# Kernel optimization log

Measured on AMD Instinct MI355X. Metric: run time of the kernel, lower is better.

The kernel has to match this reference:

```python
import jax, jax.numpy as jnp
import numpy as np
from jax import lax

COMMITMENT_WEIGHT = 0.25
EMA_DECAY = 0.99
EPS = 1e-5


def setup_inputs() -> dict:
    key = jax.random.key(0)
    k1, k2, k3 = jax.random.split(key, 3)
    B, L, D, K = 32, 512, 384, 8192
    z = jax.random.normal(k1, (B, L, D), dtype=jnp.float32)
    codebook = jax.random.normal(k2, (K, D), dtype=jnp.float32)
    ema_cluster_size = jnp.zeros((K,), dtype=jnp.float32)
    ema_embed_sum = jax.random.normal(k3, (K, D), dtype=jnp.float32)
    return {"z": z, "codebook": codebook, "ema_cluster_size": ema_cluster_size, "ema_embed_sum": ema_embed_sum}


def reference(z, codebook, ema_cluster_size, ema_embed_sum):
    B, L, D = z.shape
    K = codebook.shape[0]
    flat_z = z.reshape(-1, D)  # [N, D]

    # squared L2 distance to every code: [N, K]
    dist = (
        jnp.sum(flat_z * flat_z, axis=-1, keepdims=True)
        + jnp.sum(codebook * codebook, axis=-1)[None, :]
        - 2.0 * (flat_z @ codebook.T)
    )
    indices = jnp.argmin(dist, axis=-1)  # [N]
    quantized = codebook[indices].reshape(B, L, D)

    # EMA codebook update (training-mode, no-grad in original)
    cluster_size = jax.ops.segment_sum(jnp.ones_like(indices, dtype=flat_z.dtype), indices, num_segments=K)
    embed_sum = jax.ops.segment_sum(flat_z, indices, num_segments=K)  # [K, D]
    new_cluster_size = ema_cluster_size * EMA_DECAY + (1.0 - EMA_DECAY) * cluster_size
    new_embed_sum = ema_embed_sum * EMA_DECAY + (1.0 - EMA_DECAY) * embed_sum
    n = jnp.sum(new_cluster_size)
    cluster_size_smoothed = (new_cluster_size + EPS) / (n + K * EPS) * n
    new_codebook = new_embed_sum / cluster_size_smoothed[:, None]

    commitment_loss = jnp.mean((z - lax.stop_gradient(quantized)) ** 2)
    codebook_loss = jnp.mean((quantized - lax.stop_gradient(z)) ** 2)
    loss = codebook_loss + COMMITMENT_WEIGHT * commitment_loss

    # straight-through estimator
    quantized_st = z + lax.stop_gradient(quantized - z)
    return (quantized_st, indices.reshape(B, L), loss, new_cluster_size, new_embed_sum, new_codebook)
```

## Files before the change

kernel.cpp:

```cpp
#include <hip/hip_runtime.h>
#include <math.h>

#define N_TOK 16384
#define DDIM  384
#define KCODE 8192
#define EMA   0.99f
#define EPS_F 1e-5f
#define MARGIN 0.5f
#define NB 32

typedef _Float16 f16x8 __attribute__((ext_vector_type(8)));
typedef float    f32x4 __attribute__((ext_vector_type(4)));

#define OFF_PD1    0UL
#define OFF_PI1    2097152UL
#define OFF_PFL    4194304UL
#define OFF_CBH    6291456UL
#define OFF_TOKL   0UL
#define OFF_OFFS   65536UL
#define OFF_CURS   98560UL
#define OFF_WSIDX  12582912UL
#define OFF_COUNTS 12648448UL
#define OFF_SUMSQ  12681216UL
#define OFF_NACC   12681220UL
#define OFF_CNORM  12681472UL
#define OFF_FLIST  12714240UL
#define OFF_FCNT   12779776UL
#define OFF_PSUM   12780032UL
#define OFF_FD1    12796416UL

typedef __attribute__((address_space(1))) const unsigned int gas_uint;
typedef __attribute__((address_space(3))) unsigned int       las_uint;
__device__ __forceinline__ void gload_lds16(const void* g, void* l) {
    __builtin_amdgcn_global_load_lds((gas_uint*)g, (las_uint*)l, 16, 0, 0);
}

__global__ void convert_norm_kernel(const float* __restrict__ z, const float* __restrict__ cb,
                                    _Float16* __restrict__ zh, _Float16* __restrict__ cbh,
                                    float* __restrict__ cnorm,
                                    float* __restrict__ zero_cnts, int* __restrict__ fcnt) {
    if (blockIdx.x == 0) {
        for (int i = threadIdx.x; i < 8256; i += 256) zero_cnts[i] = 0.f;
        if (threadIdx.x < 64) fcnt[threadIdx.x] = 0;
    }
    int row  = (blockIdx.x * blockDim.x + threadIdx.x) >> 6;
    int lane = threadIdx.x & 63;
    const float* src;
    _Float16* dst;
    bool is_cb = (row >= N_TOK);
    if (is_cb) { int k = row - N_TOK; src = cb + (size_t)k * DDIM; dst = cbh + (size_t)k * DDIM; }
    else       {                      src = z  + (size_t)row * DDIM; dst = zh + (size_t)row * DDIM; }
    float s = 0.f;
    #pragma unroll
    for (int r = 0; r < 3; r++) {
        int e = (lane + 64 * r) * 2;
        float2 v = *(const float2*)(src + e);
        s = fmaf(v.x, v.x, fmaf(v.y, v.y, s));
        _Float16 h0 = (_Float16)v.x, h1 = (_Float16)v.y;
        dst[e] = h0; dst[e + 1] = h1;
    }
    if (is_cb) {
        #pragma unroll
        for (int off = 32; off > 0; off >>= 1) s += __shfl_down(s, off, 64);
        if (lane == 0) cnorm[row - N_TOK] = s;
    }
}

__launch_bounds__(512, 4)
__global__ void argmin16_kernel(const _Float16* __restrict__ zh, const _Float16* __restrict__ cbh,
                                const float* __restrict__ cnorm,
                                float* __restrict__ pd1, int* __restrict__ pi1,
                                int* __restrict__ pfl) {
    __shared__ _Float16 As[128 * 64];
    __shared__ _Float16 Bs[256 * 64];

    const int tid  = threadIdx.x;
    const int lane = tid & 63;
    const int wv   = tid >> 6;
    const int wy   = wv >> 2;
    const int wx   = wv & 3;
    const int m0   = blockIdx.x * 128;
    const int n0   = blockIdx.y * 256;
    const int l15  = lane & 15;
    const int l4   = lane >> 4;
    const int rsw  = l15 & 7;

    f32x4 acc[4][4];
    #pragma unroll
    for (int i = 0; i < 4; i++)
        #pragma unroll
        for (int j = 0; j < 4; j++) acc[i][j] = (f32x4){0.f, 0.f, 0.f, 0.f};

    const int r8  = lane >> 3;
    const int jch = (lane & 7) ^ (r8 & 7);
    const _Float16* a_g = zh  + (size_t)(m0 + wv * 8 + r8) * DDIM + jch * 8;
    const _Float16* b_g = cbh + (size_t)(n0 + wv * 8 + r8) * DDIM + jch * 8;
    _Float16* a_d = As + wv * 512;
    _Float16* b_d = Bs + wv * 512;

    gload_lds16(a_g,                      a_d);
    gload_lds16(a_g + (size_t)64 * DDIM,  a_d + 4096);
    gload_lds16(b_g,                      b_d);
    gload_lds16(b_g + (size_t)64 * DDIM,  b_d + 4096);
    gload_lds16(b_g + (size_t)128 * DDIM, b_d + 8192);
    gload_lds16(b_g + (size_t)192 * DDIM, b_d + 12288);

    for (int it = 0; it < 6; it++) {
        __syncthreads();
        f16x8 af[4], bf[4];
        #pragma unroll
        for (int im = 0; im < 4; im++)
            af[im] = *(const f16x8*)(As + (wy * 64 + im * 16 + l15) * 64 + (l4 ^ rsw) * 8);
        #pragma unroll
        for (int in = 0; in < 4; in++)
            bf[in] = *(const f16x8*)(Bs + (wx * 64 + in * 16 + l15) * 64 + (l4 ^ rsw) * 8);
        #pragma unroll
        for (int im = 0; im < 4; im++)
            #pragma unroll
            for (int in = 0; in < 4; in++)
                acc[im][in] = __builtin_amdgcn_mfma_f32_16x16x32_f16(af[im], bf[in], acc[im][in], 0, 0, 0);
        #pragma unroll
        for (int im = 0; im < 4; im++)
            af[im] = *(const f16x8*)(As + (wy * 64 + im * 16 + l15) * 64 + ((4 + l4) ^ rsw) * 8);
        #pragma unroll
        for (int in = 0; in < 4; in++)
            bf[in] = *(const f16x8*)(Bs + (wx * 64 + in * 16 + l15) * 64 + ((4 + l4) ^ rsw) * 8);
        __syncthreads();
        if (it < 5) {
            int kc = (it + 1) * 64;
            gload_lds16(a_g + kc,                      a_d);
            gload_lds16(a_g + (size_t)64 * DDIM + kc,  a_d + 4096);
            gload_lds16(b_g + kc,                      b_d);
            gload_lds16(b_g + (size_t)64 * DDIM + kc,  b_d + 4096);
            gload_lds16(b_g + (size_t)128 * DDIM + kc, b_d + 8192);
            gload_lds16(b_g + (size_t)192 * DDIM + kc, b_d + 12288);
        }
        #pragma unroll
        for (int im = 0; im < 4; im++)
            #pragma unroll
            for (int in = 0; in < 4; in++)
                acc[im][in] = __builtin_amdgcn_mfma_f32_16x16x32_f16(af[im], bf[in], acc[im][in], 0, 0, 0);
    }

    float* xd1 = (float*)&As[0];
    int*   xfl = (int*)(xd1 + 512);
    int*   xi1 = (int*)(xd1 + 1024);

    float cn[4]; int cid[4];
    #pragma unroll
    for (int in = 0; in < 4; in++) {
        cid[in] = n0 + wx * 64 + in * 16 + l15;
        cn[in] = cnorm[cid[in]];
    }
    #pragma unroll
    for (int im = 0; im < 4; im++) {
        #pragma unroll
        for (int reg = 0; reg < 4; reg++) {
            float dd[4];
            #pragma unroll
            for (int in = 0; in < 4; in++) dd[in] = cn[in] - 2.f * acc[im][in][reg];
            float d1 = dd[0]; int i1 = cid[0];
            #pragma unroll
            for (int in = 1; in < 4; in++)
                if (dd[in] < d1) { d1 = dd[in]; i1 = cid[in]; }
            #pragma unroll
            for (int off = 1; off < 16; off <<= 1) {
                float od = __shfl_xor(d1, off, 16);
                int   oi = __shfl_xor(i1, off, 16);
                if (od < d1 || (od == d1 && oi < i1)) { d1 = od; i1 = oi; }
            }
            bool fl = false;
            #pragma unroll
            for (int in = 0; in < 4; in++) fl |= (dd[in] < d1 + MARGIN) && (cid[in] != i1);
            unsigned long long bal = __ballot(fl);
            int gf = ((bal >> (l4 * 16)) & 0xFFFFULL) != 0ULL;
            if (l15 == 0) {
                int tl = wy * 64 + im * 16 + l4 * 4 + reg;
                xd1[tl * 4 + wx] = d1; xi1[tl * 4 + wx] = i1; xfl[tl * 4 + wx] = gf;
            }
        }
    }
    __syncthreads();
    if (tid < 128) {
        float d1 = xd1[tid * 4]; int i1 = xi1[tid * 4]; int fl = xfl[tid * 4];
        #pragma unroll
        for (int x = 1; x < 4; x++) {
            float od = xd1[tid * 4 + x]; int oi = xi1[tid * 4 + x]; int ofl = xfl[tid * 4 + x];
            if (od < d1 || (od == d1 && oi < i1)) { d1 = od; i1 = oi; fl = ofl; }
        }
        #pragma unroll
        for (int x = 0; x < 4; x++) {
            float od = xd1[tid * 4 + x]; int oi = xi1[tid * 4 + x];
            fl |= (oi != i1 && od < d1 + MARGIN) ? 1 : 0;
        }
        size_t o = (size_t)blockIdx.y * N_TOK + m0 + tid;
        pd1[o] = d1; pi1[o] = i1; pfl[o] = fl;
    }
}

__global__ void topmerge_kernel(const float* __restrict__ pd1, const int* __restrict__ pi1,
                                const int* __restrict__ pfl,
                                int* __restrict__ ws_idx, float* __restrict__ out_idx,
                                int* __restrict__ fcnt, int* __restrict__ flist,
                                float* __restrict__ fd1) {
    int t = blockIdx.x * blockDim.x + threadIdx.x;
    if (t >= N_TOK) return;
    float d1 = pd1[t]; int i1 = pi1[t]; int fl = pfl[t];
    float d2 = 3.4e38f;
    for (int nb = 1; nb < NB; nb++) {
        size_t o = (size_t)nb * N_TOK + t;
        float od1 = pd1[o]; int oi1 = pi1[o]; int ofl = pfl[o];
        if (od1 < d1 || (od1 == d1 && oi1 < i1)) { d2 = fminf(d2, d1); d1 = od1; i1 = oi1; fl = ofl; }
        else d2 = fminf(d2, od1);
    }
    ws_idx[t] = i1;
    out_idx[t] = (float)i1;
    fd1[t] = d1;
    if (fl || (d2 - d1 < MARGIN)) {
        int s = atomicAdd(fcnt, 1);
        flist[s] = t;
    }
}

__launch_bounds__(256)
__global__ void rescore2_kernel(const float* __restrict__ z, const float* __restrict__ cb,
                                const float* __restrict__ cnorm,
                                const float* __restrict__ pd1, const float* __restrict__ fd1,
                                const int* __restrict__ flist, const int* __restrict__ fcnt,
                                int* __restrict__ ws_idx, float* __restrict__ out_idx) {
    __shared__ float zt[4 * 384];
    const int lane = threadIdx.x & 63;
    const int wv   = threadIdx.x >> 6;
    const int count = fcnt[0];
    float* zrow = zt + wv * 384;
    for (int slot = blockIdx.x * 4 + wv; slot < count; slot += 2048 * 4) {
        int t = flist[slot];
        const float* zr = z + (size_t)t * DDIM;
        #pragma unroll
        for (int r = 0; r < 6; r++) zrow[lane + 64 * r] = zr[lane + 64 * r];
        float band = fd1[t] + MARGIN;
        float bd = 3.4e38f; int bi = 0x7fffffff;
        for (int nb = 0; nb < NB; nb++) {
            if (pd1[(size_t)nb * N_TOK + t] >= band) continue;
            #pragma unroll
            for (int c4 = 0; c4 < 4; c4++) {
                int c = nb * 256 + c4 * 64 + lane;
                const float* cr = cb + (size_t)c * DDIM;
                float a = 0.f;
                for (int d4 = 0; d4 < 96; d4++) {
                    float4 cv = *(const float4*)(cr + d4 * 4);
                    float4 zv = *(const float4*)(zrow + d4 * 4);
                    a = fmaf(zv.x, cv.x, a);
                    a = fmaf(zv.y, cv.y, a);
                    a = fmaf(zv.z, cv.z, a);
                    a = fmaf(zv.w, cv.w, a);
                }
                float dd = cnorm[c] - 2.f * a;
                if (dd < bd) { bd = dd; bi = c; }
            }
        }
        #pragma unroll
        for (int off = 32; off > 0; off >>= 1) {
            float od = __shfl_xor(bd, off, 64);
            int   oi = __shfl_xor(bi, off, 64);
            if (od < bd || (od == bd && oi < bi)) { bd = od; bi = oi; }
        }
        if (lane == 0) { ws_idx[t] = bi; out_idx[t] = (float)bi; }
    }
}

__global__ void quantize_kernel(const float* __restrict__ z, const float* __restrict__ cb,
                                const int* __restrict__ ws_idx,
                                float* __restrict__ out_q,
                                float* __restrict__ counts, float* __restrict__ psum) {
    __shared__ float sm[4];
    int t = (blockIdx.x * blockDim.x + threadIdx.x) >> 6;
    int lane = threadIdx.x & 63, wv = threadIdx.x >> 6;
    int k = ws_idx[t];
    const float* zr = z + (size_t)t * DDIM;
    const float* cr = cb + (size_t)k * DDIM;
    float* qr = out_q + (size_t)t * DDIM;
    float s = 0.f;
    #pragma unroll
    for (int r = 0; r < 6; r++) {
        int d = lane + 64 * r;
        float zv = zr[d];
        float qv = cr[d];
        qr[d] = qv;
        float df = zv - qv;
        s += df * df;
    }
    #pragma unroll
    for (int off = 32; off > 0; off >>= 1) s += __shfl_down(s, off, 64);
    if (lane == 0) {
        sm[wv] = s;
        atomicAdd(counts + k, 1.0f);
    }
    __syncthreads();
    if (threadIdx.x == 0) psum[blockIdx.x] = sm[0] + sm[1] + sm[2] + sm[3];
}

__global__ void scan_cluster_kernel(const float* __restrict__ counts,
                                    const float* __restrict__ ema_cs,
                                    const float* __restrict__ psum,
                                    int* __restrict__ offs, int* __restrict__ curs,
                                    float* __restrict__ out_ncs, float* __restrict__ n_acc,
                                    float* __restrict__ out_loss) {
    __shared__ int ps[1024];
    __shared__ float red[32];
    const int t = threadIdx.x;
    const int base = t * 8;
    int loc[8]; int s = 0; float cf[8];
    #pragma unroll
    for (int i = 0; i < 8; i++) { cf[i] = counts[base + i]; int c = (int)(cf[i] + 0.5f); loc[i] = s; s += c; }
    ps[t] = s;
    __syncthreads();
    for (int off = 1; off < 1024; off <<= 1) {
        int v = ps[t];
        int add = (t >= off) ? ps[t - off] : 0;
        __syncthreads();
        ps[t] = v + add;
        __syncthreads();
    }
    int excl = (t == 0) ? 0 : ps[t - 1];
    #pragma unroll
    for (int i = 0; i < 8; i++) {
        int o = excl + loc[i];
        offs[base + i] = o;
        curs[base + i] = o;
    }
    if (t == 1023) offs[KCODE] = ps[1023];
    float vs = 0.f;
    #pragma unroll
    for (int i = 0; i < 8; i++) {
        float v = EMA * ema_cs[base + i] + (1.f - EMA) * cf[i];
        out_ncs[base + i] = v;
        vs += v;
    }
    float ls = 0.f;
    for (int j = t; j < 4096; j += 1024) ls += psum[j];
    int lane = t & 63, w = t >> 6;
    #pragma unroll
    for (int off = 32; off > 0; off >>= 1) { vs += __shfl_down(vs, off, 64); ls += __shfl_down(ls, off, 64); }
    if (lane == 0) { red[w] = vs; red[16 + w] = ls; }
    __syncthreads();
    if (t == 0) {
        float n = 0.f, l = 0.f;
        #pragma unroll
        for (int w2 = 0; w2 < 16; w2++) { n += red[w2]; l += red[16 + w2]; }
        n_acc[0] = n;
        out_loss[0] = 1.25f * l / (float)(N_TOK * DDIM);
    }
}

__global__ void fill_kernel(const int* __restrict__ ws_idx,
                            int* __restrict__ curs, int* __restrict__ toklist) {
    int t = blockIdx.x * blockDim.x + threadIdx.x;
    if (t >= N_TOK) return;
    int k = ws_idx[t];
    int slot = atomicAdd(curs + k, 1);
    toklist[slot] = t;
}

__global__ void codebook_fused_kernel(const float* __restrict__ z,
                                      const int* __restrict__ offs, const int* __restrict__ toklist,
                                      const float* __restrict__ ema_es,
                                      const float* __restrict__ ncs, const float* __restrict__ n_acc,
                                      float* __restrict__ out_es, float* __restrict__ out_cb) {
    int k = (blockIdx.x * blockDim.x + threadIdx.x) >> 6;
    int lane = threadIdx.x & 63;
    if (k >= KCODE) return;
    int o0 = offs[k], o1 = offs[k + 1];
    float sum[6] = {0.f, 0.f, 0.f, 0.f, 0.f, 0.f};
    for (int s = o0; s < o1; s++) {
        int tok = toklist[s];
        const float* zr = z + (size_t)tok * DDIM;
        #pragma unroll
        for (int r = 0; r < 6; r++) sum[r] += zr[lane + 64 * r];
    }
    float n = n_acc[0];
    float smooth = (ncs[k] + EPS_F) / (n + (float)KCODE * EPS_F) * n;
    float inv = 1.f / smooth;
    const float* er = ema_es + (size_t)k * DDIM;
    float* oes = out_es + (size_t)k * DDIM;
    float* ocb = out_cb + (size_t)k * DDIM;
    #pragma unroll
    for (int r = 0; r < 6; r++) {
        int d = lane + 64 * r;
        float es = EMA * er[d] + (1.f - EMA) * sum[r];
        oes[d] = es;
        ocb[d] = es * inv;
    }
}

extern "C" void kernel_launch(void* const* d_in, const int* in_sizes, int n_in,
                              void* d_out, int out_size, void* d_ws, size_t ws_size,
                              hipStream_t stream) {
    const float* z       = (const float*)d_in[0];
    const float* cb      = (const float*)d_in[1];
    const float* ema_cs  = (const float*)d_in[2];
    const float* ema_es  = (const float*)d_in[3];

    float* out      = (float*)d_out;
    float* out_q    = out;
    float* out_idx  = out + 6291456;
    float* out_loss = out + 6307840;
    float* out_ncs  = out + 6307841;
    float* out_es   = out + 6316033;
    float* out_cb   = out + 9461761;

    char* w = (char*)d_ws;
    float* pd1    = (float*)(w + OFF_PD1);
    int*   pi1    = (int*)  (w + OFF_PI1);
    int*   pfl    = (int*)  (w + OFF_PFL);
    _Float16* cbh = (_Float16*)(w + OFF_CBH);
    int*   toklist= (int*)  (w + OFF_TOKL);
    int*   offs   = (int*)  (w + OFF_OFFS);
    int*   curs   = (int*)  (w + OFF_CURS);
    float* cnorm  = (float*)(w + OFF_CNORM);
    int*   flist  = (int*)  (w + OFF_FLIST);
    int*   fcnt   = (int*)  (w + OFF_FCNT);
    int*   ws_idx = (int*)  (w + OFF_WSIDX);
    float* counts = (float*)(w + OFF_COUNTS);
    float* psum   = (float*)(w + OFF_PSUM);
    float* n_acc  = (float*)(w + OFF_NACC);
    float* fd1    = (float*)(w + OFF_FD1);

    _Float16* zh = (_Float16*)out;

    convert_norm_kernel<<<(N_TOK + KCODE) / 4, 256, 0, stream>>>(z, cb, zh, cbh, cnorm, counts, fcnt);

    dim3 grid_am(N_TOK / 128, KCODE / 256, 1);
    argmin16_kernel<<<grid_am, 512, 0, stream>>>(zh, cbh, cnorm, pd1, pi1, pfl);

    topmerge_kernel<<<N_TOK / 256, 256, 0, stream>>>(pd1, pi1, pfl, ws_idx, out_idx, fcnt, flist, fd1);

    rescore2_kernel<<<2048, 256, 0, stream>>>(z, cb, cnorm, pd1, fd1, flist, fcnt, ws_idx, out_idx);

    quantize_kernel<<<N_TOK * 64 / 256, 256, 0, stream>>>(z, cb, ws_idx, out_q, counts, psum);
    scan_cluster_kernel<<<1, 1024, 0, stream>>>(counts, ema_cs, psum, offs, curs, out_ncs, n_acc, out_loss);
    fill_kernel<<<N_TOK / 256, 256, 0, stream>>>(ws_idx, curs, toklist);
    codebook_fused_kernel<<<KCODE * 64 / 256, 256, 0, stream>>>(z, offs, toklist, ema_es, out_ncs, n_acc, out_es, out_cb);
}
```

Measured before the change: 550.7 us.

## Fold quantize pass into codebook update and move counts into argmin merge

Removes the separate quantize kernel. Cluster counts are now accumulated with atomics in topmerge for unflagged tokens and in rescore for flagged ones. The quantized output write and the loss sum of squares move into the per-code codebook kernel, which already reads each assigned token's z row, so z is read once fewer. The loss is zeroed in scan and then accumulated with atomics, which makes its summation order nondeterministic. Work per code is now uneven, since codes with many tokens also write all of their quantized rows.

```diff
diff --git a/kernel.cpp b/kernel.cpp
--- a/kernel.cpp
+++ b/kernel.cpp
@@ -26,7 +26,6 @@
 #define OFF_CNORM  12681472UL
 #define OFF_FLIST  12714240UL
 #define OFF_FCNT   12779776UL
-#define OFF_PSUM   12780032UL
 #define OFF_FD1    12796416UL
 
 typedef __attribute__((address_space(1))) const unsigned int gas_uint;
@@ -202,7 +201,7 @@
                                 const int* __restrict__ pfl,
                                 int* __restrict__ ws_idx, float* __restrict__ out_idx,
                                 int* __restrict__ fcnt, int* __restrict__ flist,
-                                float* __restrict__ fd1) {
+                                float* __restrict__ fd1, float* __restrict__ counts) {
     int t = blockIdx.x * blockDim.x + threadIdx.x;
     if (t >= N_TOK) return;
     float d1 = pd1[t]; int i1 = pi1[t]; int fl = pfl[t];
@@ -219,6 +218,8 @@
     if (fl || (d2 - d1 < MARGIN)) {
         int s = atomicAdd(fcnt, 1);
         flist[s] = t;
+    } else {
+        atomicAdd(counts + i1, 1.0f);
     }
 }
 
@@ -227,7 +228,8 @@
                                 const float* __restrict__ cnorm,
                                 const float* __restrict__ pd1, const float* __restrict__ fd1,
                                 const int* __restrict__ flist, const int* __restrict__ fcnt,
-                                int* __restrict__ ws_idx, float* __restrict__ out_idx) {
+                                int* __restrict__ ws_idx, float* __restrict__ out_idx,
+                                float* __restrict__ counts) {
     __shared__ float zt[4 * 384];
     const int lane = threadIdx.x & 63;
     const int wv   = threadIdx.x >> 6;
@@ -265,49 +267,20 @@
             int   oi = __shfl_xor(bi, off, 64);
             if (od < bd || (od == bd && oi < bi)) { bd = od; bi = oi; }
         }
-        if (lane == 0) { ws_idx[t] = bi; out_idx[t] = (float)bi; }
-    }
-}
-
-__global__ void quantize_kernel(const float* __restrict__ z, const float* __restrict__ cb,
-                                const int* __restrict__ ws_idx,
-                                float* __restrict__ out_q,
-                                float* __restrict__ counts, float* __restrict__ psum) {
-    __shared__ float sm[4];
-    int t = (blockIdx.x * blockDim.x + threadIdx.x) >> 6;
-    int lane = threadIdx.x & 63, wv = threadIdx.x >> 6;
-    int k = ws_idx[t];
-    const float* zr = z + (size_t)t * DDIM;
-    const float* cr = cb + (size_t)k * DDIM;
-    float* qr = out_q + (size_t)t * DDIM;
-    float s = 0.f;
-    #pragma unroll
-    for (int r = 0; r < 6; r++) {
-        int d = lane + 64 * r;
-        float zv = zr[d];
-        float qv = cr[d];
-        qr[d] = qv;
-        float df = zv - qv;
-        s += df * df;
-    }
-    #pragma unroll
-    for (int off = 32; off > 0; off >>= 1) s += __shfl_down(s, off, 64);
-    if (lane == 0) {
-        sm[wv] = s;
-        atomicAdd(counts + k, 1.0f);
-    }
-    __syncthreads();
-    if (threadIdx.x == 0) psum[blockIdx.x] = sm[0] + sm[1] + sm[2] + sm[3];
+        if (lane == 0) {
+            ws_idx[t] = bi; out_idx[t] = (float)bi;
+            atomicAdd(counts + bi, 1.0f);
+        }
+    }
 }
 
 __global__ void scan_cluster_kernel(const float* __restrict__ counts,
                                     const float* __restrict__ ema_cs,
-                                    const float* __restrict__ psum,
                                     int* __restrict__ offs, int* __restrict__ curs,
                                     float* __restrict__ out_ncs, float* __restrict__ n_acc,
                                     float* __restrict__ out_loss) {
     __shared__ int ps[1024];
-    __shared__ float red[32];
+    __shared__ float red[16];
     const int t = threadIdx.x;
     const int base = t * 8;
     int loc[8]; int s = 0; float cf[8];
@@ -337,19 +310,17 @@
         out_ncs[base + i] = v;
         vs += v;
     }
-    float ls = 0.f;
-    for (int j = t; j < 4096; j += 1024) ls += psum[j];
     int lane = t & 63, w = t >> 6;
     #pragma unroll
-    for (int off = 32; off > 0; off >>= 1) { vs += __shfl_down(vs, off, 64); ls += __shfl_down(ls, off, 64); }
-    if (lane == 0) { red[w] = vs; red[16 + w] = ls; }
+    for (int off = 32; off > 0; off >>= 1) vs += __shfl_down(vs, off, 64);
+    if (lane == 0) red[w] = vs;
     __syncthreads();
     if (t == 0) {
-        float n = 0.f, l = 0.f;
-        #pragma unroll
-        for (int w2 = 0; w2 < 16; w2++) { n += red[w2]; l += red[16 + w2]; }
+        float n = 0.f;
+        #pragma unroll
+        for (int w2 = 0; w2 < 16; w2++) n += red[w2];
         n_acc[0] = n;
-        out_loss[0] = 1.25f * l / (float)(N_TOK * DDIM);
+        out_loss[0] = 0.f;
     }
 }
 
@@ -362,34 +333,59 @@
     toklist[slot] = t;
 }
 
-__global__ void codebook_fused_kernel(const float* __restrict__ z,
+__global__ void codebook_fused_kernel(const float* __restrict__ z, const float* __restrict__ cb,
                                       const int* __restrict__ offs, const int* __restrict__ toklist,
                                       const float* __restrict__ ema_es,
                                       const float* __restrict__ ncs, const float* __restrict__ n_acc,
-                                      float* __restrict__ out_es, float* __restrict__ out_cb) {
+                                      float* __restrict__ out_q, float* __restrict__ out_es,
+                                      float* __restrict__ out_cb, float* __restrict__ out_loss) {
+    __shared__ float sm[4];
     int k = (blockIdx.x * blockDim.x + threadIdx.x) >> 6;
     int lane = threadIdx.x & 63;
-    if (k >= KCODE) return;
-    int o0 = offs[k], o1 = offs[k + 1];
-    float sum[6] = {0.f, 0.f, 0.f, 0.f, 0.f, 0.f};
-    for (int s = o0; s < o1; s++) {
-        int tok = toklist[s];
-        const float* zr = z + (size_t)tok * DDIM;
-        #pragma unroll
-        for (int r = 0; r < 6; r++) sum[r] += zr[lane + 64 * r];
-    }
-    float n = n_acc[0];
-    float smooth = (ncs[k] + EPS_F) / (n + (float)KCODE * EPS_F) * n;
-    float inv = 1.f / smooth;
-    const float* er = ema_es + (size_t)k * DDIM;
-    float* oes = out_es + (size_t)k * DDIM;
-    float* ocb = out_cb + (size_t)k * DDIM;
-    #pragma unroll
-    for (int r = 0; r < 6; r++) {
-        int d = lane + 64 * r;
-        float es = EMA * er[d] + (1.f - EMA) * sum[r];
-        oes[d] = es;
-        ocb[d] = es * inv;
+    int wv = threadIdx.x >> 6;
+    float sumsq = 0.f;
+    if (k < KCODE) {
+        int o0 = offs[k], o1 = offs[k + 1];
+        float ck[6];
+        const float* cr = cb + (size_t)k * DDIM;
+        #pragma unroll
+        for (int r = 0; r < 6; r++) ck[r] = cr[lane + 64 * r];
+        float sum[6] = {0.f, 0.f, 0.f, 0.f, 0.f, 0.f};
+        for (int s = o0; s < o1; s++) {
+            int tok = toklist[s];
+            const float* zr = z + (size_t)tok * DDIM;
+            float* qr = out_q + (size_t)tok * DDIM;
+            #pragma unroll
+            for (int r = 0; r < 6; r++) {
+                int d = lane + 64 * r;
+                float zv = zr[d];
+                sum[r] += zv;
+                float df = zv - ck[r];
+                sumsq = fmaf(df, df, sumsq);
+                qr[d] = ck[r];
+            }
+        }
+        float n = n_acc[0];
+        float smooth = (ncs[k] + EPS_F) / (n + (float)KCODE * EPS_F) * n;
+        float inv = 1.f / smooth;
+        const float* er = ema_es + (size_t)k * DDIM;
+        float* oes = out_es + (size_t)k * DDIM;
+        float* ocb = out_cb + (size_t)k * DDIM;
+        #pragma unroll
+        for (int r = 0; r < 6; r++) {
+            int d = lane + 64 * r;
+            float es = EMA * er[d] + (1.f - EMA) * sum[r];
+            oes[d] = es;
+            ocb[d] = es * inv;
+        }
+    }
+    #pragma unroll
+    for (int off = 32; off > 0; off >>= 1) sumsq += __shfl_down(sumsq, off, 64);
+    if (lane == 0) sm[wv] = sumsq;
+    __syncthreads();
+    if (threadIdx.x == 0) {
+        float b = sm[0] + sm[1] + sm[2] + sm[3];
+        atomicAdd(out_loss, 1.25f * b / (float)(N_TOK * DDIM));
     }
 }
 
@@ -422,7 +418,6 @@
     int*   fcnt   = (int*)  (w + OFF_FCNT);
     int*   ws_idx = (int*)  (w + OFF_WSIDX);
     float* counts = (float*)(w + OFF_COUNTS);
-    float* psum   = (float*)(w + OFF_PSUM);
     float* n_acc  = (float*)(w + OFF_NACC);
     float* fd1    = (float*)(w + OFF_FD1);
 
@@ -433,12 +428,12 @@
     dim3 grid_am(N_TOK / 128, KCODE / 256, 1);
     argmin16_kernel<<<grid_am, 512, 0, stream>>>(zh, cbh, cnorm, pd1, pi1, pfl);
 
-    topmerge_kernel<<<N_TOK / 256, 256, 0, stream>>>(pd1, pi1, pfl, ws_idx, out_idx, fcnt, flist, fd1);
-
-    rescore2_kernel<<<2048, 256, 0, stream>>>(z, cb, cnorm, pd1, fd1, flist, fcnt, ws_idx, out_idx);
-
-    quantize_kernel<<<N_TOK * 64 / 256, 256, 0, stream>>>(z, cb, ws_idx, out_q, counts, psum);
-    scan_cluster_kernel<<<1, 1024, 0, stream>>>(counts, ema_cs, psum, offs, curs, out_ncs, n_acc, out_loss);
+    topmerge_kernel<<<N_TOK / 256, 256, 0, stream>>>(pd1, pi1, pfl, ws_idx, out_idx, fcnt, flist, fd1, counts);
+
+    rescore2_kernel<<<2048, 256, 0, stream>>>(z, cb, cnorm, pd1, fd1, flist, fcnt, ws_idx, out_idx, counts);
+
+    scan_cluster_kernel<<<1, 1024, 0, stream>>>(counts, ema_cs, offs, curs, out_ncs, n_acc, out_loss);
     fill_kernel<<<N_TOK / 256, 256, 0, stream>>>(ws_idx, curs, toklist);
-    codebook_fused_kernel<<<KCODE * 64 / 256, 256, 0, stream>>>(z, offs, toklist, ema_es, out_ncs, n_acc, out_es, out_cb);
-}
+    codebook_fused_kernel<<<KCODE * 64 / 256, 256, 0, stream>>>(z, cb, offs, toklist, ema_es, out_ncs, n_acc,
+                                                                out_q, out_es, out_cb, out_loss);
+}
```

Measured after the change: 569.9 us. 1.03x slower.
